# Performance work log

Measured on AMD Instinct MI355X. Metric: run time of the kernel, lower is better.

## Reference

```python
import jax, jax.numpy as jnp
import numpy as np

ROPE_BASE = 10000.0


def _apply_rope(x, positions):
    # x: [B, S, H, Dh], positions: [S]
    d_head = x.shape[-1]
    half = d_head // 2
    inv_freq = 1.0 / (ROPE_BASE ** (jnp.arange(0, half, dtype=jnp.float32) * 2.0 / d_head))
    angles = positions.astype(jnp.float32)[:, None] * inv_freq[None, :]  # [S, half]
    cos = jnp.cos(angles)[None, :, None, :]  # [1,S,1,half]
    sin = jnp.sin(angles)[None, :, None, :]
    x1, x2 = jnp.split(x, 2, axis=-1)
    return jnp.concatenate([x1 * cos - x2 * sin, x1 * sin + x2 * cos], axis=-1)


def _alibi_slopes(n_heads):
    # standard ALiBi slopes: 2^(-8*(h+1)/n_heads)
    return 2.0 ** (-8.0 * (jnp.arange(1, n_heads + 1, dtype=jnp.float32) / n_heads))


def setup_inputs() -> dict:
    key = jax.random.key(0)
    ks = jax.random.split(key, 5)
    B, S, D = 2, 2048, 2048
    H, KVH, Dh = 16, 4, 128
    std = 0.02
    return {
        "residual": jax.random.normal(ks[0], (B, S, D), dtype=jnp.float32),
        "W_Q": jax.random.normal(ks[1], (H, Dh, D), dtype=jnp.float32) * std,
        "W_K": jax.random.normal(ks[2], (KVH, Dh, D), dtype=jnp.float32) * std,
        "W_V": jax.random.normal(ks[3], (KVH, Dh, D), dtype=jnp.float32) * std,
        "W_O": jax.random.normal(ks[4], (H, Dh, D), dtype=jnp.float32) * std,
        "start_pos": 0,
    }


def reference(residual, W_Q, W_K, W_V, W_O, start_pos):
    B, S, D = residual.shape
    H, Dh, _ = W_Q.shape
    KVH = W_K.shape[0]
    # projections (prefill path: cache=None, total_len == S)
    q = jnp.einsum('bsd,hed->bshe', residual, W_Q)   # [B,S,H,Dh]
    k = jnp.einsum('bsd,hed->bshe', residual, W_K)   # [B,S,KVH,Dh]
    v = jnp.einsum('bsd,hed->bshe', residual, W_V)   # [B,S,KVH,Dh]
    # RoPE
    positions = start_pos + jnp.arange(S)
    q = _apply_rope(q, positions)
    k = _apply_rope(k, positions)
    k_for_cache = k
    v_for_cache = v
    # GQA head repeat
    rep = H // KVH
    k_r = jnp.repeat(k, rep, axis=2)
    v_r = jnp.repeat(v, rep, axis=2)
    # attention scores [B,H,Sq,Sk]
    scores = jnp.einsum('bqhe,bkhe->bhqk', q, k_r) / jnp.sqrt(jnp.float32(Dh))
    # ALiBi bias (sliced rows start_pos:start_pos+S of the total_len x total_len bias)
    slopes = _alibi_slopes(H)  # [H]
    qpos = start_pos + jnp.arange(S)
    kpos = jnp.arange(S)
    bias = -slopes[:, None, None] * (qpos[:, None] - kpos[None, :]).astype(jnp.float32)
    scores = scores + bias[None, :, :, :]
    # causal mask: keep j <= i (tril of ones)
    mask = kpos[None, :] <= qpos[:, None]  # with start_pos=0 this is tril
    scores = jnp.where(mask[None, None, :, :], scores, -jnp.inf)
    pattern = jax.nn.softmax(scores, axis=-1)
    attn = jnp.einsum('bhqk,bkhe->bqhe', pattern, v_r)
    output = jnp.einsum('bqhe,hed->bqd', attn, W_O)
    return output, k_for_cache, v_for_cache
```

## Files before the change

kernel.cpp:

```cpp
#include <hip/hip_runtime.h>


typedef __attribute__((ext_vector_type(8))) short frag8;
typedef __attribute__((ext_vector_type(4))) float facc4;

#define DEVI __device__ __forceinline__

constexpr int Bc  = 2;
constexpr int Sc  = 2048;
constexpr int Dc  = 2048;
constexpr int Hc  = 16;
constexpr int KVHc = 4;
constexpr int Dhc = 128;
constexpr int Mc  = Bc * Sc;
constexpr int NQc = Hc * Dhc;
constexpr int NKVc = KVHc * Dhc;

DEVI unsigned short f2bf(float f) {
  union { float f; unsigned u; } v; v.f = f;
  return (unsigned short)((v.u + 0x7fffu + ((v.u >> 16) & 1u)) >> 16);
}
DEVI float bf2f(unsigned short h) {
  union { unsigned u; float f; } v; v.u = ((unsigned)h) << 16;
  return v.f;
}

DEVI void gload_lds16(const void* g, void* l) {
  __builtin_amdgcn_global_load_lds(
      (const __attribute__((address_space(1))) unsigned int*)g,
      (__attribute__((address_space(3))) unsigned int*)l, 16, 0, 0);
}

DEVI float rowred_max(float x) {
  union { float f; int i; } a, b;
  a.f = x;
  b.i = __builtin_amdgcn_update_dpp(a.i, a.i, 0x128, 0xF, 0xF, false); a.f = fmaxf(a.f, b.f);
  b.i = __builtin_amdgcn_update_dpp(a.i, a.i, 0x124, 0xF, 0xF, false); a.f = fmaxf(a.f, b.f);
  b.i = __builtin_amdgcn_update_dpp(a.i, a.i, 0x122, 0xF, 0xF, false); a.f = fmaxf(a.f, b.f);
  b.i = __builtin_amdgcn_update_dpp(a.i, a.i, 0x121, 0xF, 0xF, false); a.f = fmaxf(a.f, b.f);
  return a.f;
}
DEVI float rowred_sum(float x) {
  union { float f; int i; } a, b;
  a.f = x;
  b.i = __builtin_amdgcn_update_dpp(a.i, a.i, 0x128, 0xF, 0xF, false); a.f += b.f;
  b.i = __builtin_amdgcn_update_dpp(a.i, a.i, 0x124, 0xF, 0xF, false); a.f += b.f;
  b.i = __builtin_amdgcn_update_dpp(a.i, a.i, 0x122, 0xF, 0xF, false); a.f += b.f;
  b.i = __builtin_amdgcn_update_dpp(a.i, a.i, 0x121, 0xF, 0xF, false); a.f += b.f;
  return a.f;
}


__global__ void cvt_all(const float* __restrict__ residual,
                        const float* __restrict__ WQ,
                        const float* __restrict__ WK,
                        const float* __restrict__ WV,
                        const float* __restrict__ WO,
                        unsigned short* __restrict__ rb,
                        unsigned short* __restrict__ wqb,
                        unsigned short* __restrict__ wkvb,
                        unsigned short* __restrict__ wob) {
  __shared__ float tile[64][65];
  int bid = blockIdx.x;
  int t = threadIdx.x;
  if (bid < 14336) {
    const float* src; unsigned short* dst; int off;
    if (bid < 8192)       { src = residual; dst = rb;  off = bid; }
    else if (bid < 12288) { src = WQ; dst = wqb; off = bid - 8192; }
    else if (bid < 13312) { src = WK; dst = wkvb; off = bid - 12288; }
    else                  { src = WV; dst = wkvb + (size_t)NKVc * Dc; off = bid - 13312; }
    int i = (off * 256 + t) * 4;
    float4 v = *(const float4*)(src + i);
    ushort4 o;
    o.x = f2bf(v.x); o.y = f2bf(v.y); o.z = f2bf(v.z); o.w = f2bf(v.w);
    *(ushort4*)(dst + i) = o;
  } else {
    int tb = bid - 14336;
    int r0 = (tb >> 5) * 64;
    int c0 = (tb & 31) * 64;
#pragma unroll
    for (int i = 0; i < 16; ++i) {
      int idx = i * 256 + t; int r = idx >> 6, c = idx & 63;
      tile[r][c] = WO[(size_t)(r0 + r) * Dc + c0 + c];
    }
    __syncthreads();
#pragma unroll
    for (int i = 0; i < 16; ++i) {
      int idx = i * 256 + t; int r = idx >> 6, c = idx & 63;
      wob[(size_t)(c0 + r) * NQc + r0 + c] = f2bf(tile[c][r]);
    }
  }
}


template <int MODE>
__global__ __launch_bounds__(256) void gemm_nt(
    const unsigned short* __restrict__ Amat,
    const unsigned short* __restrict__ Bmat,
    float* __restrict__ Cf, float* __restrict__ Cf2,
    unsigned short* __restrict__ Cb,
    int Nn, int Kk) {
  __shared__ __align__(16) unsigned short As[128 * 32];
  __shared__ __align__(16) unsigned short Bs[128 * 32];
  int t = threadIdx.x;
  int lane = t & 63, w = t >> 6;
  int quad = lane >> 4, l16 = lane & 15;
  int wm = (w >> 1) * 64, wn = (w & 1) * 64;
  int m0 = blockIdx.x * 128, n0 = blockIdx.y * 128;

  facc4 acc[4][4] = {};

  const int nIter = Kk / 32;
  for (int kt = 0; kt < nIter; ++kt) {
    __syncthreads();
#pragma unroll
    for (int i = 0; i < 2; ++i) {
      int c = i * 256 + t;
      int row = c >> 2, ch = c & 3;
      gload_lds16(Amat + (size_t)(m0 + row) * Kk + kt * 32 + ch * 8, &As[c * 8]);
      gload_lds16(Bmat + (size_t)(n0 + row) * Kk + kt * 32 + ch * 8, &Bs[c * 8]);
    }
    asm volatile("s_waitcnt vmcnt(0)" ::: "memory");
    __syncthreads();

    frag8 aF[4], bF[4];
#pragma unroll
    for (int mi = 0; mi < 4; ++mi)
      aF[mi] = *(const frag8*)&As[(wm + mi * 16 + l16) * 32 + quad * 8];
#pragma unroll
    for (int ni = 0; ni < 4; ++ni)
      bF[ni] = *(const frag8*)&Bs[(wn + ni * 16 + l16) * 32 + quad * 8];
#pragma unroll
    for (int mi = 0; mi < 4; ++mi)
#pragma unroll
      for (int ni = 0; ni < 4; ++ni)
        acc[mi][ni] = __builtin_amdgcn_mfma_f32_16x16x32_bf16(
            aF[mi], bF[ni], acc[mi][ni], 0, 0, 0);
  }

#pragma unroll
  for (int mi = 0; mi < 4; ++mi)
#pragma unroll
    for (int ni = 0; ni < 4; ++ni)
#pragma unroll
      for (int i = 0; i < 4; ++i) {
        int mrow = m0 + wm + mi * 16 + quad * 4 + i;
        int ncol = n0 + wn + ni * 16 + l16;
        float v = acc[mi][ni][i];
        if (MODE == 0) {
          Cf[(size_t)mrow * Nn + ncol] = v;
        } else if (MODE == 1) {
          Cb[(size_t)mrow * Nn + ncol] = f2bf(v);
        } else {
          if (ncol < NKVc) {
            Cf[(size_t)mrow * NKVc + ncol] = v;
          } else {
            int nc = ncol - NKVc;
            Cf2[(size_t)mrow * NKVc + nc] = v;
            int b = mrow >> 11, s = mrow & (Sc - 1);
            Cb[((size_t)(b * NKVc + nc)) * Sc + s] = f2bf(v);
          }
        }
      }
}


__global__ void rope_all(unsigned short* qb, float* kf, unsigned short* kb,
                         const int* __restrict__ sp) {
  int idx = blockIdx.x * 256 + threadIdx.x;
  constexpr int NQ = Mc * Hc * 64;
  if (idx < NQ) {
    int e = idx & 63, h = (idx >> 6) & 15, m = idx >> 10;
    int s = m & (Sc - 1);
    float pos = (float)(sp[0] + s);
    float invf = exp2f(-(float)e * 0.20762050593046835f);
    float ang = pos * invf;
    float sn, cs; sincosf(ang, &sn, &cs);
    size_t base = (size_t)m * NQc + h * Dhc + e;
    float x1 = bf2f(qb[base]), x2 = bf2f(qb[base + 64]);
    qb[base]      = f2bf(x1 * cs - x2 * sn);
    qb[base + 64] = f2bf(x1 * sn + x2 * cs);
  } else {
    int j = idx - NQ;
    int e = j & 63, kvh = (j >> 6) & 3, m = j >> 8;
    int s = m & (Sc - 1);
    float pos = (float)(sp[0] + s);
    float invf = exp2f(-(float)e * 0.20762050593046835f);
    float ang = pos * invf;
    float sn, cs; sincosf(ang, &sn, &cs);
    size_t base = (size_t)m * NKVc + kvh * Dhc + e;
    float x1 = kf[base], x2 = kf[base + 64];
    float o1 = x1 * cs - x2 * sn;
    float o2 = x1 * sn + x2 * cs;
    kf[base] = o1; kf[base + 64] = o2;
    kb[base] = f2bf(o1); kb[base + 64] = f2bf(o2);
  }
}


DEVI void issue_tile(const unsigned short* kb, const unsigned short* vbT,
                     int bb, int kvh, int kt, int t,
                     unsigned short* KsB, unsigned short* VtB) {
#pragma unroll
  for (int i = 0; i < 4; ++i) {
    int c = i * 256 + t;
    int row = c >> 4, chp = c & 15;
    int ch = chp ^ (row & 15);
    gload_lds16(kb + (size_t)(bb * Sc + kt * 64 + row) * NKVc + kvh * Dhc + ch * 8,
                KsB + c * 8);
  }
#pragma unroll
  for (int i = 0; i < 4; ++i) {
    int c = i * 256 + t;
    int row = c >> 3, chp = c & 7;
    int ch = chp ^ (row & 7);
    gload_lds16(vbT + ((size_t)(bb * KVHc + kvh) * Dhc + row) * Sc + kt * 64 + ch * 8,
                VtB + c * 8);
  }
}

DEVI void load_q(frag8 (&aQc)[4], const unsigned short* qb, int bb, int qt,
                 int h, int w, int quad, int l16) {
  const unsigned short* qrow =
      qb + (size_t)(bb * Sc + qt * 64 + w * 16 + l16) * NQc + h * Dhc;
#pragma unroll
  for (int kd = 0; kd < 4; ++kd)
    aQc[kd] = *(const frag8*)(qrow + (kd * 4 + quad) * 8);
}

DEVI void write_o(unsigned short* qb, facc4 (&oacc)[8], float (&lrow)[4],
                  int bb, int qt, int h, int w, int quad, int l16) {
  float rinv[4];
#pragma unroll
  for (int i = 0; i < 4; ++i) rinv[i] = 1.0f / rowred_sum(lrow[i]);
#pragma unroll
  for (int c8 = 0; c8 < 8; ++c8)
#pragma unroll
    for (int i = 0; i < 4; ++i) {
      int row = qt * 64 + w * 16 + quad * 4 + i;
      size_t o = ((size_t)(bb * Sc + row) * Hc + h) * Dhc + c8 * 16 + l16;
      qb[o] = f2bf(oacc[c8][i] * rinv[i]);
    }
}

__global__ __launch_bounds__(256, 2) void flash_attn(
    unsigned short* qb,
    const unsigned short* __restrict__ kb,
    const unsigned short* __restrict__ vbT,
    const int* __restrict__ spp) {
  __shared__ __align__(16) unsigned short Ks[2][64 * 128];
  __shared__ __align__(16) unsigned short Vt[2][128 * 64];
  __shared__ __align__(16) unsigned short Ps[4][16 * 64];

  int g = blockIdx.x & 7;
  int bb = g >> 2, kvh = g & 3;
  int inner = blockIdx.x >> 3;
  int pair = inner & 15, hh = inner >> 4;
  int h = kvh * 4 + hh;
  int qtA = pair, qtB = 31 - pair;

  int t = threadIdx.x, lane = t & 63, w = t >> 6;
  int quad = lane >> 4, l16 = lane & 15;
  int sp = spp[0];
  constexpr float LOG2E = 1.4426950408889634f;
  const float SC = 0.08838834764831845f * LOG2E;
  float slope2 = exp2f(-0.5f * (float)(h + 1)) * LOG2E;
  float s2x16 = slope2 * 16.0f;
  float s2x64 = slope2 * 64.0f;

  int tA = min((sp + qtA * 64 + 63) >> 6, 31) + 1;
  int tB = min((sp + qtB * 64 + 63) >> 6, 31) + 1;
  int total = tA + tB;

  frag8 aQc[4];
  load_q(aQc, qb, bb, qtA, h, w, quad, l16);

  facc4 oacc[8] = {};
  float mrow[4], lrow[4], bq[4], adn[4][4];
  int qposi[4];
  int qt = qtA;
#pragma unroll
  for (int i = 0; i < 4; ++i) {
    mrow[i] = -1e30f; lrow[i] = 0.f;
    qposi[i] = sp + qt * 64 + w * 16 + quad * 4 + i;
    bq[i] = slope2 * (float)qposi[i];
  }

  issue_tile(kb, vbT, bb, kvh, tA - 1, t, Ks[0], Vt[0]);

  for (int it = 0; it < total; ++it) {
    if (it == tA) {
      write_o(qb, oacc, lrow, bb, qtA, h, w, quad, l16);
      load_q(aQc, qb, bb, qtB, h, w, quad, l16);
      qt = qtB;
#pragma unroll
      for (int c8 = 0; c8 < 8; ++c8)
#pragma unroll
        for (int i = 0; i < 4; ++i) oacc[c8][i] = 0.f;
#pragma unroll
      for (int i = 0; i < 4; ++i) {
        mrow[i] = -1e30f; lrow[i] = 0.f;
        qposi[i] = sp + qt * 64 + w * 16 + quad * 4 + i;
        bq[i] = slope2 * (float)qposi[i];
      }
    }
    int kt = (it < tA) ? (tA - 1 - it) : (total - 1 - it);
    bool first = (it == 0) || (it == tA);

    if (it + 1 < total) {
      int nk = (it + 1 < tA) ? (tA - 2 - it) : (total - 2 - it);
      issue_tile(kb, vbT, bb, kvh, nk, t, Ks[(it + 1) & 1], Vt[(it + 1) & 1]);
      asm volatile("s_waitcnt vmcnt(8)" ::: "memory");
    } else {
      asm volatile("s_waitcnt vmcnt(0)" ::: "memory");
    }
    __builtin_amdgcn_s_barrier();
    asm volatile("" ::: "memory");

    const unsigned short* KsB = Ks[it & 1];
    const unsigned short* VtB = Vt[it & 1];

    facc4 sacc[4] = {};
#pragma unroll
    for (int kd = 0; kd < 4; ++kd) {
      int ch = kd * 4 + quad;
#pragma unroll
      for (int c4 = 0; c4 < 4; ++c4) {
        frag8 bK = *(const frag8*)&KsB[(c4 * 16 + l16) * 128 + (ch ^ l16) * 8];
        sacc[c4] = __builtin_amdgcn_mfma_f32_16x16x32_bf16(aQc[kd], bK, sacc[c4], 0, 0, 0);
      }
    }

    unsigned short* Pw = &Ps[w][0];
    int r0 = quad * 4;
    bool needmask = (kt * 64 + 63) > (sp + qt * 64);

    if (first || needmask) {
      float sv[4][4];
      float mt[4] = {-1e30f, -1e30f, -1e30f, -1e30f};
#pragma unroll
      for (int c4 = 0; c4 < 4; ++c4) {
        int kpos = kt * 64 + c4 * 16 + l16;
        float bk = slope2 * (float)kpos;
#pragma unroll
        for (int i = 0; i < 4; ++i) {
          float v = fmaf(sacc[c4][i], SC, bk - bq[i]);
          if (needmask) v = (kpos <= qposi[i]) ? v : -1e30f;
          sv[c4][i] = v;
          mt[i] = fmaxf(mt[i], v);
        }
      }
#pragma unroll
      for (int i = 0; i < 4; ++i) mt[i] = rowred_max(mt[i]);
#pragma unroll
      for (int i = 0; i < 4; ++i) {
        float mn = fmaxf(mrow[i], mt[i]);
        float alpha = exp2f(mrow[i] - mn);
        mrow[i] = mn;
        lrow[i] *= alpha;
#pragma unroll
        for (int c8 = 0; c8 < 8; ++c8) oacc[c8][i] *= alpha;
      }
#pragma unroll
      for (int c4 = 0; c4 < 4; ++c4) {
        float p0 = exp2f(sv[c4][0] - mrow[0]);
        float p1 = exp2f(sv[c4][1] - mrow[1]);
        float p2 = exp2f(sv[c4][2] - mrow[2]);
        float p3 = exp2f(sv[c4][3] - mrow[3]);
        lrow[0] += p0; lrow[1] += p1; lrow[2] += p2; lrow[3] += p3;
        unsigned u01, u23;
        asm("v_cvt_pk_bf16_f32 %0, %1, %2" : "=v"(u01) : "v"(p0), "v"(p1));
        asm("v_cvt_pk_bf16_f32 %0, %1, %2" : "=v"(u23) : "v"(p2), "v"(p3));
        int kk = c4 * 16 + l16;
        int col = kk & 7, chnk = kk >> 3;
        Pw[(r0 + 0) * 64 + ((chnk ^ ((r0 + 0) & 7)) * 8) + col] = (unsigned short)(u01 & 0xffffu);
        Pw[(r0 + 1) * 64 + ((chnk ^ ((r0 + 1) & 7)) * 8) + col] = (unsigned short)(u01 >> 16);
        Pw[(r0 + 2) * 64 + ((chnk ^ ((r0 + 2) & 7)) * 8) + col] = (unsigned short)(u23 & 0xffffu);
        Pw[(r0 + 3) * 64 + ((chnk ^ ((r0 + 3) & 7)) * 8) + col] = (unsigned short)(u23 >> 16);
      }
      float bkn0 = slope2 * (float)((kt - 1) * 64 + l16);
#pragma unroll
      for (int c4 = 0; c4 < 4; ++c4) {
        float bkc = bkn0 + (float)c4 * s2x16;
#pragma unroll
        for (int i = 0; i < 4; ++i) adn[c4][i] = bkc - bq[i] - mrow[i];
      }
    } else {
#pragma unroll
      for (int c4 = 0; c4 < 4; ++c4) {
        float p0 = exp2f(fmaf(sacc[c4][0], SC, adn[c4][0]));
        float p1 = exp2f(fmaf(sacc[c4][1], SC, adn[c4][1]));
        float p2 = exp2f(fmaf(sacc[c4][2], SC, adn[c4][2]));
        float p3 = exp2f(fmaf(sacc[c4][3], SC, adn[c4][3]));
        lrow[0] += p0; lrow[1] += p1; lrow[2] += p2; lrow[3] += p3;
        adn[c4][0] -= s2x64; adn[c4][1] -= s2x64;
        adn[c4][2] -= s2x64; adn[c4][3] -= s2x64;
        unsigned u01, u23;
        asm("v_cvt_pk_bf16_f32 %0, %1, %2" : "=v"(u01) : "v"(p0), "v"(p1));
        asm("v_cvt_pk_bf16_f32 %0, %1, %2" : "=v"(u23) : "v"(p2), "v"(p3));
        int kk = c4 * 16 + l16;
        int col = kk & 7, chnk = kk >> 3;
        Pw[(r0 + 0) * 64 + ((chnk ^ ((r0 + 0) & 7)) * 8) + col] = (unsigned short)(u01 & 0xffffu);
        Pw[(r0 + 1) * 64 + ((chnk ^ ((r0 + 1) & 7)) * 8) + col] = (unsigned short)(u01 >> 16);
        Pw[(r0 + 2) * 64 + ((chnk ^ ((r0 + 2) & 7)) * 8) + col] = (unsigned short)(u23 & 0xffffu);
        Pw[(r0 + 3) * 64 + ((chnk ^ ((r0 + 3) & 7)) * 8) + col] = (unsigned short)(u23 >> 16);
      }
    }

#pragma unroll
    for (int k2 = 0; k2 < 2; ++k2) {
      int ch = k2 * 4 + quad;
      frag8 aP = *(const frag8*)&Ps[w][l16 * 64 + (ch ^ (l16 & 7)) * 8];
#pragma unroll
      for (int c8 = 0; c8 < 8; ++c8) {
        frag8 bV = *(const frag8*)&VtB[(c8 * 16 + l16) * 64 + (ch ^ (l16 & 7)) * 8];
        oacc[c8] = __builtin_amdgcn_mfma_f32_16x16x32_bf16(aP, bV, oacc[c8], 0, 0, 0);
      }
    }

    if (!first) {
      int ovf = (lrow[0] > 16777216.f) || (lrow[1] > 16777216.f) ||
                (lrow[2] > 16777216.f) || (lrow[3] > 16777216.f);
      if (__any(ovf)) {
        const float DS = 0x1p-32f;
#pragma unroll
        for (int i = 0; i < 4; ++i) { lrow[i] *= DS; mrow[i] += 32.f; }
#pragma unroll
        for (int c4 = 0; c4 < 4; ++c4)
#pragma unroll
          for (int i = 0; i < 4; ++i) adn[c4][i] -= 32.f;
#pragma unroll
        for (int c8 = 0; c8 < 8; ++c8)
#pragma unroll
          for (int i = 0; i < 4; ++i) oacc[c8][i] *= DS;
      }
    }

    asm volatile("" ::: "memory");
    __builtin_amdgcn_s_barrier();
  }

  write_o(qb, oacc, lrow, bb, qtB, h, w, quad, l16);
}


extern "C" void kernel_launch(void* const* d_in, const int* in_sizes, int n_in,
                              void* d_out, int out_size, void* d_ws, size_t ws_size,
                              hipStream_t stream) {
  const float* residual = (const float*)d_in[0];
  const float* W_Q = (const float*)d_in[1];
  const float* W_K = (const float*)d_in[2];
  const float* W_V = (const float*)d_in[3];
  const float* W_O = (const float*)d_in[4];
  const int* start_pos = (const int*)d_in[5];

  float* out = (float*)d_out;
  float* kf = out + (size_t)Bc * Sc * Dc;
  float* vf = kf + (size_t)Mc * NKVc;

  char* w = (char*)d_ws;
  auto alloc = [&](size_t bytes) {
    char* p = w; w += (bytes + 255) & ~(size_t)255; return p;
  };
  unsigned short* rb   = (unsigned short*)alloc((size_t)Mc * Dc * 2);
  unsigned short* wqb  = (unsigned short*)alloc((size_t)NQc * Dc * 2);
  unsigned short* wkvb = (unsigned short*)alloc((size_t)2 * NKVc * Dc * 2);
  unsigned short* wob  = (unsigned short*)alloc((size_t)Dc * NQc * 2);
  unsigned short* qb   = (unsigned short*)alloc((size_t)Mc * NQc * 2);
  unsigned short* kb   = (unsigned short*)alloc((size_t)Mc * NKVc * 2);
  unsigned short* vbT  = (unsigned short*)alloc((size_t)Mc * NKVc * 2);
  (void)ws_size; (void)in_sizes; (void)n_in; (void)out_size;

  cvt_all<<<15360, 256, 0, stream>>>(residual, W_Q, W_K, W_V, W_O,
                                     rb, wqb, wkvb, wob);

  gemm_nt<1><<<dim3(32, 16), 256, 0, stream>>>(rb, wqb, nullptr, nullptr, qb, NQc, Dc);
  gemm_nt<2><<<dim3(32, 8), 256, 0, stream>>>(rb, wkvb, kf, vf, vbT, 2 * NKVc, Dc);

  rope_all<<<20480, 256, 0, stream>>>(qb, kf, kb, start_pos);

  flash_attn<<<512, 256, 0, stream>>>(qb, kb, vbT, start_pos);

  gemm_nt<0><<<dim3(32, 16), 256, 0, stream>>>(qb, wob, out, nullptr, nullptr, Dc, Dc);
}
```

Baseline: 365.6 us.

## Replace GEMMs with 256x128 double-buffered 8-wave pipelined kernel and fuse QKV projection

Swaps the simple single-buffered 128x128 GEMM for a 256x128-tile, 512-thread kernel. It double-buffers LDS, XOR-swizzles the LDS layout, and interleaves global-to-LDS loads for the next K tiles with MFMA phases, using barriers and s_setprio. The Q and K/V projections are merged into one GEMM over a concatenated weight buffer, with the epilogue routing columns to the Q, K and V outputs. This targets load-latency stalls, LDS bank conflicts and launch count, at the cost of heavier barrier use and more complex hand scheduling of waitcnts.

```diff
diff --git a/kernel.cpp b/kernel.cpp
--- a/kernel.cpp
+++ b/kernel.cpp
@@ -30,6 +30,9 @@
       (const __attribute__((address_space(1))) unsigned int*)g,
       (__attribute__((address_space(3))) unsigned int*)l, 16, 0, 0);
 }
+
+#define MEMBAR() asm volatile("" ::: "memory")
+#define FULLBAR() do { MEMBAR(); __builtin_amdgcn_s_barrier(); MEMBAR(); } while (0)
 
 DEVI float rowred_max(float x) {
   union { float f; int i; } a, b;
@@ -93,72 +96,149 @@
 }
 
 
+DEVI void stageA8(const unsigned short* A, unsigned short* lds,
+                  int m0, int kt, int hf, int t, int Kk) {
+#pragma unroll
+  for (int s = 0; s < 2; ++s) {
+    int c = s * 512 + t;
+    int x = c * 16;
+    int g = x ^ ((((unsigned)x >> 9) & 1) << 5);
+    int row = g >> 7, colb = g & 127;
+    gload_lds16(A + (size_t)(m0 + hf * 128 + row) * Kk + kt * 64 + (colb >> 1),
+                lds + hf * 8192 + c * 8);
+  }
+}
+DEVI void stageB8(const unsigned short* B, unsigned short* lds,
+                  int n0, int kt, int hf, int t, int Kk) {
+  int c = t;
+  int x = c * 16;
+  int g = x ^ ((((unsigned)x >> 9) & 1) << 5);
+  int row = g >> 7, colb = g & 127;
+  gload_lds16(B + (size_t)(n0 + hf * 64 + row) * Kk + kt * 64 + (colb >> 1),
+              lds + hf * 4096 + c * 8);
+}
+
 template <int MODE>
-__global__ __launch_bounds__(256) void gemm_nt(
+__global__ __launch_bounds__(512, 2) void gemm8p(
     const unsigned short* __restrict__ Amat,
     const unsigned short* __restrict__ Bmat,
     float* __restrict__ Cf, float* __restrict__ Cf2,
-    unsigned short* __restrict__ Cb,
+    unsigned short* __restrict__ Cb, unsigned short* __restrict__ Cb2,
     int Nn, int Kk) {
-  __shared__ __align__(16) unsigned short As[128 * 32];
-  __shared__ __align__(16) unsigned short Bs[128 * 32];
+  __shared__ __align__(16) unsigned short As[2][256 * 64];
+  __shared__ __align__(16) unsigned short Bs[2][128 * 64];
+
   int t = threadIdx.x;
   int lane = t & 63, w = t >> 6;
   int quad = lane >> 4, l16 = lane & 15;
-  int wm = (w >> 1) * 64, wn = (w & 1) * 64;
-  int m0 = blockIdx.x * 128, n0 = blockIdx.y * 128;
-
-  facc4 acc[4][4] = {};
-
-  const int nIter = Kk / 32;
-  for (int kt = 0; kt < nIter; ++kt) {
-    __syncthreads();
-#pragma unroll
-    for (int i = 0; i < 2; ++i) {
-      int c = i * 256 + t;
-      int row = c >> 2, ch = c & 3;
-      gload_lds16(Amat + (size_t)(m0 + row) * Kk + kt * 32 + ch * 8, &As[c * 8]);
-      gload_lds16(Bmat + (size_t)(n0 + row) * Kk + kt * 32 + ch * 8, &Bs[c * 8]);
-    }
-    asm volatile("s_waitcnt vmcnt(0)" ::: "memory");
-    __syncthreads();
-
-    frag8 aF[4], bF[4];
-#pragma unroll
-    for (int mi = 0; mi < 4; ++mi)
-      aF[mi] = *(const frag8*)&As[(wm + mi * 16 + l16) * 32 + quad * 8];
-#pragma unroll
-    for (int ni = 0; ni < 4; ++ni)
-      bF[ni] = *(const frag8*)&Bs[(wn + ni * 16 + l16) * 32 + quad * 8];
-#pragma unroll
-    for (int mi = 0; mi < 4; ++mi)
-#pragma unroll
-      for (int ni = 0; ni < 4; ++ni)
-        acc[mi][ni] = __builtin_amdgcn_mfma_f32_16x16x32_bf16(
-            aF[mi], bF[ni], acc[mi][ni], 0, 0, 0);
-  }
-
-#pragma unroll
-  for (int mi = 0; mi < 4; ++mi)
-#pragma unroll
-    for (int ni = 0; ni < 4; ++ni)
+  int wm = (w >> 2) * 128;
+  int wn = (w & 3) * 32;
+  int m0 = blockIdx.x * 256, n0 = blockIdx.y * 128;
+  const int NT = Kk >> 6;
+
+  unsigned swz = ((l16 >> 2) & 1) << 5;
+  auto aoff = [&](int mi, int ks) {
+    return ((((wm + mi * 16 + l16) * 128) + ks * 64 + quad * 16) ^ swz) >> 1;
+  };
+  auto boff = [&](int nf, int ks) {
+    return ((((wn + nf * 16 + l16) * 128) + ks * 64 + quad * 16) ^ swz) >> 1;
+  };
+
+  stageA8(Amat, As[0], m0, 0, 0, t, Kk);
+  stageA8(Amat, As[0], m0, 0, 1, t, Kk);
+  stageB8(Bmat, Bs[0], n0, 0, 0, t, Kk);
+  stageB8(Bmat, Bs[0], n0, 0, 1, t, Kk);
+  stageA8(Amat, As[1], m0, 1, 0, t, Kk);
+  stageA8(Amat, As[1], m0, 1, 1, t, Kk);
+  asm volatile("s_waitcnt vmcnt(4)" ::: "memory");
+  FULLBAR();
+
+  facc4 acc[8][2] = {};
+
+  for (int kt = 0; kt < NT; ++kt) {
+    const int p = kt & 1;
+    const unsigned short* Ab = As[p];
+    const unsigned short* Bb = Bs[p];
+    unsigned short* Anx = As[p];
+    unsigned short* Bnx = Bs[1 - p];
+    frag8 aF[8][2];
+    frag8 bf00, bf01, bf10, bf11;
+
+#pragma unroll
+    for (int mi = 0; mi < 8; ++mi) aF[mi][0] = *(const frag8*)&Ab[aoff(mi, 0)];
+    bf00 = *(const frag8*)&Bb[boff(0, 0)];
+    if (kt + 1 < NT) stageB8(Bmat, Bnx, n0, kt + 1, 0, t, Kk);
+    FULLBAR();
+    asm volatile("s_waitcnt lgkmcnt(0)" ::: "memory");
+    __builtin_amdgcn_s_setprio(1);
+#pragma unroll
+    for (int mi = 0; mi < 8; ++mi)
+      acc[mi][0] = __builtin_amdgcn_mfma_f32_16x16x32_bf16(aF[mi][0], bf00, acc[mi][0], 0, 0, 0);
+    __builtin_amdgcn_s_setprio(0);
+    FULLBAR();
+
+#pragma unroll
+    for (int mi = 0; mi < 8; ++mi) aF[mi][1] = *(const frag8*)&Ab[aoff(mi, 1)];
+    bf01 = *(const frag8*)&Bb[boff(0, 1)];
+    if (kt + 1 < NT) stageB8(Bmat, Bnx, n0, kt + 1, 1, t, Kk);
+    FULLBAR();
+    asm volatile("s_waitcnt lgkmcnt(0)" ::: "memory");
+    __builtin_amdgcn_s_setprio(1);
+#pragma unroll
+    for (int mi = 0; mi < 8; ++mi)
+      acc[mi][0] = __builtin_amdgcn_mfma_f32_16x16x32_bf16(aF[mi][1], bf01, acc[mi][0], 0, 0, 0);
+    __builtin_amdgcn_s_setprio(0);
+    FULLBAR();
+
+    bf10 = *(const frag8*)&Bb[boff(1, 0)];
+    if (kt + 2 < NT) stageA8(Amat, Anx, m0, kt + 2, 0, t, Kk);
+    FULLBAR();
+    asm volatile("s_waitcnt lgkmcnt(0)" ::: "memory");
+    __builtin_amdgcn_s_setprio(1);
+#pragma unroll
+    for (int mi = 0; mi < 8; ++mi)
+      acc[mi][1] = __builtin_amdgcn_mfma_f32_16x16x32_bf16(aF[mi][0], bf10, acc[mi][1], 0, 0, 0);
+    __builtin_amdgcn_s_setprio(0);
+    FULLBAR();
+
+    bf11 = *(const frag8*)&Bb[boff(1, 1)];
+    if (kt + 2 < NT) {
+      stageA8(Amat, Anx, m0, kt + 2, 1, t, Kk);
+      asm volatile("s_waitcnt vmcnt(4)" ::: "memory");
+    } else {
+      asm volatile("s_waitcnt vmcnt(0)" ::: "memory");
+    }
+    FULLBAR();
+    asm volatile("s_waitcnt lgkmcnt(0)" ::: "memory");
+    __builtin_amdgcn_s_setprio(1);
+#pragma unroll
+    for (int mi = 0; mi < 8; ++mi)
+      acc[mi][1] = __builtin_amdgcn_mfma_f32_16x16x32_bf16(aF[mi][1], bf11, acc[mi][1], 0, 0, 0);
+    __builtin_amdgcn_s_setprio(0);
+    FULLBAR();
+  }
+
+#pragma unroll
+  for (int mi = 0; mi < 8; ++mi)
+#pragma unroll
+    for (int nf = 0; nf < 2; ++nf)
 #pragma unroll
       for (int i = 0; i < 4; ++i) {
-        int mrow = m0 + wm + mi * 16 + quad * 4 + i;
-        int ncol = n0 + wn + ni * 16 + l16;
-        float v = acc[mi][ni][i];
+        int row = m0 + wm + mi * 16 + quad * 4 + i;
+        int col = n0 + wn + nf * 16 + l16;
+        float v = acc[mi][nf][i];
         if (MODE == 0) {
-          Cf[(size_t)mrow * Nn + ncol] = v;
-        } else if (MODE == 1) {
-          Cb[(size_t)mrow * Nn + ncol] = f2bf(v);
+          Cf[(size_t)row * Nn + col] = v;
         } else {
-          if (ncol < NKVc) {
-            Cf[(size_t)mrow * NKVc + ncol] = v;
+          if (col < NQc) {
+            Cb[(size_t)row * NQc + col] = f2bf(v);
+          } else if (col < NQc + NKVc) {
+            Cf[(size_t)row * NKVc + (col - NQc)] = v;
           } else {
-            int nc = ncol - NKVc;
-            Cf2[(size_t)mrow * NKVc + nc] = v;
-            int b = mrow >> 11, s = mrow & (Sc - 1);
-            Cb[((size_t)(b * NKVc + nc)) * Sc + s] = f2bf(v);
+            int nc = col - NQc - NKVc;
+            Cf2[(size_t)row * NKVc + nc] = v;
+            int b = row >> 11, s = row & (Sc - 1);
+            Cb2[((size_t)(b * NKVc + nc)) * Sc + s] = f2bf(v);
           }
         }
       }
@@ -463,8 +543,7 @@
     char* p = w; w += (bytes + 255) & ~(size_t)255; return p;
   };
   unsigned short* rb   = (unsigned short*)alloc((size_t)Mc * Dc * 2);
-  unsigned short* wqb  = (unsigned short*)alloc((size_t)NQc * Dc * 2);
-  unsigned short* wkvb = (unsigned short*)alloc((size_t)2 * NKVc * Dc * 2);
+  unsigned short* wqkv = (unsigned short*)alloc((size_t)(NQc + 2 * NKVc) * Dc * 2);
   unsigned short* wob  = (unsigned short*)alloc((size_t)Dc * NQc * 2);
   unsigned short* qb   = (unsigned short*)alloc((size_t)Mc * NQc * 2);
   unsigned short* kb   = (unsigned short*)alloc((size_t)Mc * NKVc * 2);
@@ -472,14 +551,15 @@
   (void)ws_size; (void)in_sizes; (void)n_in; (void)out_size;
 
   cvt_all<<<15360, 256, 0, stream>>>(residual, W_Q, W_K, W_V, W_O,
-                                     rb, wqb, wkvb, wob);
-
-  gemm_nt<1><<<dim3(32, 16), 256, 0, stream>>>(rb, wqb, nullptr, nullptr, qb, NQc, Dc);
-  gemm_nt<2><<<dim3(32, 8), 256, 0, stream>>>(rb, wkvb, kf, vf, vbT, 2 * NKVc, Dc);
+                                     rb, wqkv, wqkv + (size_t)NQc * Dc, wob);
+
+  gemm8p<1><<<dim3(16, 24), 512, 0, stream>>>(rb, wqkv, kf, vf, qb, vbT,
+                                              NQc + 2 * NKVc, Dc);
 
   rope_all<<<20480, 256, 0, stream>>>(qb, kf, kb, start_pos);
 
   flash_attn<<<512, 256, 0, stream>>>(qb, kb, vbT, start_pos);
 
-  gemm_nt<0><<<dim3(32, 16), 256, 0, stream>>>(qb, wob, out, nullptr, nullptr, Dc, Dc);
-}
+  gemm8p<0><<<dim3(16, 16), 512, 0, stream>>>(qb, wob, out, nullptr, nullptr,
+                                              nullptr, Dc, Dc);
+}
```

Result: no change. 371.4 us (+1.6%).

## Double-buffer GEMM with swizzled LDS and fuse QKV projections into one launch

Applied to the files above, without the earlier changes.

Rewrites the bf16 MFMA GEMM to use a K-tile of 64 with double-buffered LDS. The next tile's global loads are issued while the current tile is computed, and the per-iteration vmcnt wait is removed. LDS addresses are XOR-swizzled to avoid bank conflicts. The Q and KV projection GEMMs are merged into one launch over a concatenated weight buffer, which cuts a launch and improves grid fill. LDS use doubles to 64KB per block, which may limit occupancy. Dropping the explicit vmcnt wait relies on the barrier ordering to make the async LDS loads visible.

```diff
diff --git a/kernel.cpp b/kernel.cpp
--- a/kernel.cpp
+++ b/kernel.cpp
@@ -93,72 +93,103 @@
 }
 
 
+DEVI void stage_tile(const unsigned short* A, const unsigned short* B,
+                     unsigned short* Al, unsigned short* Bl,
+                     int m0, int n0, int kt, int t, int Kk) {
+#pragma unroll
+  for (int i = 0; i < 4; ++i) {
+    int c = i * 256 + t;
+    int row = c >> 3, ch = c & 7;
+    int g = ch ^ (row & 7);
+    gload_lds16(A + (size_t)(m0 + row) * Kk + kt * 64 + g * 8, Al + c * 8);
+  }
+#pragma unroll
+  for (int i = 0; i < 4; ++i) {
+    int c = i * 256 + t;
+    int row = c >> 3, ch = c & 7;
+    int g = ch ^ (row & 7);
+    gload_lds16(B + (size_t)(n0 + row) * Kk + kt * 64 + g * 8, Bl + c * 8);
+  }
+}
+
 template <int MODE>
-__global__ __launch_bounds__(256) void gemm_nt(
+__global__ __launch_bounds__(256, 2) void gemm2b(
     const unsigned short* __restrict__ Amat,
     const unsigned short* __restrict__ Bmat,
     float* __restrict__ Cf, float* __restrict__ Cf2,
-    unsigned short* __restrict__ Cb,
+    unsigned short* __restrict__ Cb, unsigned short* __restrict__ Cb2,
     int Nn, int Kk) {
-  __shared__ __align__(16) unsigned short As[128 * 32];
-  __shared__ __align__(16) unsigned short Bs[128 * 32];
+  __shared__ __align__(16) unsigned short As[2][128 * 64];
+  __shared__ __align__(16) unsigned short Bs[2][128 * 64];
+
   int t = threadIdx.x;
   int lane = t & 63, w = t >> 6;
   int quad = lane >> 4, l16 = lane & 15;
+  int l7 = l16 & 7;
   int wm = (w >> 1) * 64, wn = (w & 1) * 64;
   int m0 = blockIdx.x * 128, n0 = blockIdx.y * 128;
+  const int NT = Kk >> 6;
+
+  auto aoff = [&](int mi, int ks) {
+    return (wm + mi * 16 + l16) * 64 + (((ks * 4 + quad) ^ l7) * 8);
+  };
+  auto boff = [&](int ni, int ks) {
+    return (wn + ni * 16 + l16) * 64 + (((ks * 4 + quad) ^ l7) * 8);
+  };
+
+  stage_tile(Amat, Bmat, As[0], Bs[0], m0, n0, 0, t, Kk);
+  __syncthreads();
 
   facc4 acc[4][4] = {};
 
-  const int nIter = Kk / 32;
-  for (int kt = 0; kt < nIter; ++kt) {
+  for (int kt = 0; kt < NT; ++kt) {
+    const int p = kt & 1;
+    if (kt + 1 < NT)
+      stage_tile(Amat, Bmat, As[1 - p], Bs[1 - p], m0, n0, kt + 1, t, Kk);
+
+    const unsigned short* Ab = As[p];
+    const unsigned short* Bb = Bs[p];
+    frag8 aFr[4][2], bFr[4][2];
+#pragma unroll
+    for (int ks = 0; ks < 2; ++ks) {
+#pragma unroll
+      for (int mi = 0; mi < 4; ++mi) aFr[mi][ks] = *(const frag8*)&Ab[aoff(mi, ks)];
+#pragma unroll
+      for (int ni = 0; ni < 4; ++ni) bFr[ni][ks] = *(const frag8*)&Bb[boff(ni, ks)];
+    }
+#pragma unroll
+    for (int ks = 0; ks < 2; ++ks)
+#pragma unroll
+      for (int mi = 0; mi < 4; ++mi)
+#pragma unroll
+        for (int ni = 0; ni < 4; ++ni)
+          acc[mi][ni] = __builtin_amdgcn_mfma_f32_16x16x32_bf16(
+              aFr[mi][ks], bFr[ni][ks], acc[mi][ni], 0, 0, 0);
+
     __syncthreads();
-#pragma unroll
-    for (int i = 0; i < 2; ++i) {
-      int c = i * 256 + t;
-      int row = c >> 2, ch = c & 3;
-      gload_lds16(Amat + (size_t)(m0 + row) * Kk + kt * 32 + ch * 8, &As[c * 8]);
-      gload_lds16(Bmat + (size_t)(n0 + row) * Kk + kt * 32 + ch * 8, &Bs[c * 8]);
-    }
-    asm volatile("s_waitcnt vmcnt(0)" ::: "memory");
-    __syncthreads();
-
-    frag8 aF[4], bF[4];
-#pragma unroll
-    for (int mi = 0; mi < 4; ++mi)
-      aF[mi] = *(const frag8*)&As[(wm + mi * 16 + l16) * 32 + quad * 8];
+  }
+
+#pragma unroll
+  for (int mi = 0; mi < 4; ++mi)
 #pragma unroll
     for (int ni = 0; ni < 4; ++ni)
-      bF[ni] = *(const frag8*)&Bs[(wn + ni * 16 + l16) * 32 + quad * 8];
-#pragma unroll
-    for (int mi = 0; mi < 4; ++mi)
-#pragma unroll
-      for (int ni = 0; ni < 4; ++ni)
-        acc[mi][ni] = __builtin_amdgcn_mfma_f32_16x16x32_bf16(
-            aF[mi], bF[ni], acc[mi][ni], 0, 0, 0);
-  }
-
-#pragma unroll
-  for (int mi = 0; mi < 4; ++mi)
-#pragma unroll
-    for (int ni = 0; ni < 4; ++ni)
 #pragma unroll
       for (int i = 0; i < 4; ++i) {
-        int mrow = m0 + wm + mi * 16 + quad * 4 + i;
-        int ncol = n0 + wn + ni * 16 + l16;
+        int row = m0 + wm + mi * 16 + quad * 4 + i;
+        int col = n0 + wn + ni * 16 + l16;
         float v = acc[mi][ni][i];
         if (MODE == 0) {
-          Cf[(size_t)mrow * Nn + ncol] = v;
-        } else if (MODE == 1) {
-          Cb[(size_t)mrow * Nn + ncol] = f2bf(v);
+          Cf[(size_t)row * Nn + col] = v;
         } else {
-          if (ncol < NKVc) {
-            Cf[(size_t)mrow * NKVc + ncol] = v;
+          if (col < NQc) {
+            Cb[(size_t)row * NQc + col] = f2bf(v);
+          } else if (col < NQc + NKVc) {
+            Cf[(size_t)row * NKVc + (col - NQc)] = v;
           } else {
-            int nc = ncol - NKVc;
-            Cf2[(size_t)mrow * NKVc + nc] = v;
-            int b = mrow >> 11, s = mrow & (Sc - 1);
-            Cb[((size_t)(b * NKVc + nc)) * Sc + s] = f2bf(v);
+            int nc = col - NQc - NKVc;
+            Cf2[(size_t)row * NKVc + nc] = v;
+            int b = row >> 11, s = row & (Sc - 1);
+            Cb2[((size_t)(b * NKVc + nc)) * Sc + s] = f2bf(v);
           }
         }
       }
@@ -463,8 +494,7 @@
     char* p = w; w += (bytes + 255) & ~(size_t)255; return p;
   };
   unsigned short* rb   = (unsigned short*)alloc((size_t)Mc * Dc * 2);
-  unsigned short* wqb  = (unsigned short*)alloc((size_t)NQc * Dc * 2);
-  unsigned short* wkvb = (unsigned short*)alloc((size_t)2 * NKVc * Dc * 2);
+  unsigned short* wqkv = (unsigned short*)alloc((size_t)(NQc + 2 * NKVc) * Dc * 2);
   unsigned short* wob  = (unsigned short*)alloc((size_t)Dc * NQc * 2);
   unsigned short* qb   = (unsigned short*)alloc((size_t)Mc * NQc * 2);
   unsigned short* kb   = (unsigned short*)alloc((size_t)Mc * NKVc * 2);
@@ -472,14 +502,15 @@
   (void)ws_size; (void)in_sizes; (void)n_in; (void)out_size;
 
   cvt_all<<<15360, 256, 0, stream>>>(residual, W_Q, W_K, W_V, W_O,
-                                     rb, wqb, wkvb, wob);
-
-  gemm_nt<1><<<dim3(32, 16), 256, 0, stream>>>(rb, wqb, nullptr, nullptr, qb, NQc, Dc);
-  gemm_nt<2><<<dim3(32, 8), 256, 0, stream>>>(rb, wkvb, kf, vf, vbT, 2 * NKVc, Dc);
+                                     rb, wqkv, wqkv + (size_t)NQc * Dc, wob);
+
+  gemm2b<1><<<dim3(32, 24), 256, 0, stream>>>(rb, wqkv, kf, vf, qb, vbT,
+                                              NQc + 2 * NKVc, Dc);
 
   rope_all<<<20480, 256, 0, stream>>>(qb, kf, kb, start_pos);
 
   flash_attn<<<512, 256, 0, stream>>>(qb, kb, vbT, start_pos);
 
-  gemm_nt<0><<<dim3(32, 16), 256, 0, stream>>>(qb, wob, out, nullptr, nullptr, Dc, Dc);
-}
+  gemm2b<0><<<dim3(32, 16), 256, 0, stream>>>(qb, wob, out, nullptr, nullptr,
+                                              nullptr, Dc, Dc);
+}
```

After: 316.5 us. 1.16x faster.
